# Kernel optimization log

Measured on AMD Instinct MI355X. Metric: run time of the kernel, lower is better.

## Reference

```python
import jax, jax.numpy as jnp
import numpy as np

D_MODEL = 1024
N_HEADS = 16
D_HEAD = D_MODEL // N_HEADS
BATCH = 4
SEQ = 2048
NEG_INF = -1e9  # finite large-negative; avoids NaNs on fully-masked rows under jit


def setup_inputs() -> dict:
    key = jax.random.key(0)
    ks = jax.random.split(key, 10)
    xav = np.sqrt(6.0 / (D_MODEL + D_MODEL))  # xavier_uniform bound
    def w(k):
        return jax.random.uniform(k, (D_MODEL, D_MODEL), jnp.float32, -xav, xav)
    return {
        "x": jax.random.normal(ks[0], (BATCH, SEQ, D_MODEL), jnp.float32),
        "attention_mask": jnp.tril(jnp.ones((SEQ, SEQ), jnp.int32)),  # causal: 0 => masked
        "key_padding_mask": jnp.zeros((BATCH, SEQ), jnp.bool_),  # True => masked
        "Wq": w(ks[1]), "bq": jnp.zeros((D_MODEL,), jnp.float32),
        "Wk": w(ks[2]), "bk": jnp.zeros((D_MODEL,), jnp.float32),
        "Wv": w(ks[3]), "bv": jnp.zeros((D_MODEL,), jnp.float32),
        "Wo": w(ks[4]), "bo": jnp.zeros((D_MODEL,), jnp.float32),
    }


def reference(x, attention_mask, key_padding_mask, Wq, bq, Wk, bk, Wv, bv, Wo, bo):
    b, s, d = x.shape
    scale = 1.0 / np.sqrt(D_HEAD)
    # torch Linear: x @ W.T + b
    def proj(W, bias):
        y = jnp.einsum('bsd,ed->bse', x, W) + bias
        return y.reshape(b, s, N_HEADS, D_HEAD).transpose(0, 2, 1, 3)  # (b,h,s,dh)
    q = proj(Wq, bq)
    k = proj(Wk, bk)
    v = proj(Wv, bv)
    scores = jnp.einsum('bhqd,bhkd->bhqk', q, k) * scale  # (b,h,s,s)
    scores = jnp.where(attention_mask[None, None] == 0, NEG_INF, scores)
    scores = jnp.where(key_padding_mask[:, None, None, :], NEG_INF, scores)
    attn = jax.nn.softmax(scores, axis=-1)
    out = jnp.einsum('bhqk,bhkd->bhqd', attn, v)  # (b,h,s,dh)
    out = out.transpose(0, 2, 1, 3).reshape(b, s, d)
    out = jnp.einsum('bsd,ed->bse', out, Wo) + bo
    return out
```

## Files before the change

kernel.cpp:

```cpp
#include <hip/hip_runtime.h>
#include <stdint.h>

typedef __bf16 bf16;
typedef __bf16 bf16x4 __attribute__((ext_vector_type(4)));
typedef __bf16 bf16x8 __attribute__((ext_vector_type(8)));
typedef float f32x4 __attribute__((ext_vector_type(4)));

typedef __attribute__((address_space(3))) uint32_t lds_u32_t;
typedef const __attribute__((address_space(1))) uint32_t glb_u32_t;

#define MFMA16(a, b, c) __builtin_amdgcn_mfma_f32_16x16x32_bf16((a), (b), (c), 0, 0, 0)

#if __has_builtin(__builtin_amdgcn_exp2f)
#define EXP2(x) __builtin_amdgcn_exp2f(x)
#else
#define EXP2(x) exp2f(x)
#endif

#define SEQ 2048
#define DMODEL 1024
#define NH 16
#define DH 64
#define MTOT 8192

#define KVB 64

#define VMW(n) asm volatile("s_waitcnt vmcnt(" #n ")" ::: "memory")
#define LGKM0()                                         \
  {                                                     \
    asm volatile("s_waitcnt lgkmcnt(0)" ::: "memory");  \
    __builtin_amdgcn_sched_barrier(0);                  \
  }
#define BARR()                                          \
  {                                                     \
    asm volatile("" ::: "memory");                      \
    __builtin_amdgcn_s_barrier();                       \
    asm volatile("" ::: "memory");                      \
  }

__global__ __launch_bounds__(256) void cvt_all(const float* __restrict__ x,
                                               const float* __restrict__ W0,
                                               const float* __restrict__ W1,
                                               const float* __restrict__ W2,
                                               const float* __restrict__ W3,
                                               bf16* __restrict__ xo, bf16* __restrict__ o0,
                                               bf16* __restrict__ o1, bf16* __restrict__ o2,
                                               bf16* __restrict__ o3) {
  int bid = blockIdx.x;
  const float* in;
  bf16* out;
  int within;
  if (bid < 8192) {
    in = x; out = xo; within = bid;
  } else {
    int r = bid - 8192;
    int wsel = r >> 10;
    within = r & 1023;
    switch (wsel) {
      case 0: in = W0; out = o0; break;
      case 1: in = W1; out = o1; break;
      case 2: in = W2; out = o2; break;
      default: in = W3; out = o3; break;
    }
  }
  int idx = (within * 256 + threadIdx.x) * 4;
  float4 v = *reinterpret_cast<const float4*>(in + idx);
  bf16x4 o;
  o[0] = (bf16)v.x; o[1] = (bf16)v.y; o[2] = (bf16)v.z; o[3] = (bf16)v.w;
  *reinterpret_cast<bf16x4*>(out + idx) = o;
}

static __device__ __forceinline__ void stage16(const bf16* g, const bf16* l) {
  __builtin_amdgcn_global_load_lds((glb_u32_t*)g, (lds_u32_t*)l, 16, 0, 0);
}

static __device__ __forceinline__ bf16x8 frag_ld(const bf16* base, int row, int col) {
  uint32_t byte = ((uint32_t)(row * 64 + col) * 2u) ^ (uint32_t)((row & 7) << 4);
  return *reinterpret_cast<const bf16x8*>(reinterpret_cast<const char*>(base) + byte);
}

static __device__ __forceinline__ void gemm128(const bf16* __restrict__ A,
                                               const bf16* __restrict__ B, int m0, int n0,
                                               int w, int lane, bf16* As, bf16* Bs,
                                               f32x4 acc[2][4]) {
  const int wm = w >> 1, wn = w & 1;
  const int cA = lane & 15, gA = lane >> 4;
  const int r8 = lane >> 3;
  const int csw = ((lane & 7) ^ r8) << 3;

#define SA_(kk, buf)                                                               \
  {                                                                                \
    _Pragma("unroll") for (int i_ = 0; i_ < 2; ++i_) {                             \
      int ci_ = w * 2 + i_;                                                        \
      stage16(A + (size_t)(m0 + ci_ * 8 + r8) * 1024 + (kk) + csw,                 \
              As + (buf)*8192 + ci_ * 512);                                        \
    }                                                                              \
  }
#define SB_(kk, buf)                                                               \
  {                                                                                \
    _Pragma("unroll") for (int i_ = 0; i_ < 2; ++i_) {                             \
      int ci_ = w * 2 + i_;                                                        \
      stage16(B + (size_t)(n0 + ci_ * 8 + r8) * 1024 + (kk) + csw,                 \
              Bs + (buf)*8192 + ci_ * 512);                                        \
    }                                                                              \
  }
#define CL3(x) ((x) < 16 ? (x) : (x)-3)
#define CL2(x) ((x) < 16 ? (x) : (x)-2)

  SA_(0, 0)
  SB_(0, 0)
  SA_(64, 1)
  VMW(2);
  BARR();

  int cur = 0, nxt = 1, nx2 = 2;
  bf16x8 aA[2], bB[4];

  for (int t = 0; t < 16; ++t) {
    const int bcur = t & 1;
    const bf16* Ac = As + cur * 8192;
    const bf16* Bc = Bs + bcur * 8192;

#pragma unroll
    for (int mi = 0; mi < 2; ++mi) aA[mi] = frag_ld(Ac, wm * 32 + mi * 16 + cA, gA * 8);
#pragma unroll
    for (int ni = 0; ni < 4; ++ni) bB[ni] = frag_ld(Bc, wn * 64 + ni * 16 + cA, gA * 8);

    SB_(CL2(t + 1) * 64, bcur ^ 1)

    BARR();
    LGKM0();
    __builtin_amdgcn_s_setprio(1);
#pragma unroll
    for (int mi = 0; mi < 2; ++mi)
#pragma unroll
      for (int ni = 0; ni < 4; ++ni) acc[mi][ni] = MFMA16(aA[mi], bB[ni], acc[mi][ni]);
    __builtin_amdgcn_s_setprio(0);
    BARR();

#pragma unroll
    for (int mi = 0; mi < 2; ++mi) aA[mi] = frag_ld(Ac, wm * 32 + mi * 16 + cA, 32 + gA * 8);
#pragma unroll
    for (int ni = 0; ni < 4; ++ni) bB[ni] = frag_ld(Bc, wn * 64 + ni * 16 + cA, 32 + gA * 8);

    SA_(CL3(t + 2) * 64, nx2)

    VMW(2);
    BARR();
    LGKM0();
    __builtin_amdgcn_s_setprio(1);
#pragma unroll
    for (int mi = 0; mi < 2; ++mi)
#pragma unroll
      for (int ni = 0; ni < 4; ++ni) acc[mi][ni] = MFMA16(aA[mi], bB[ni], acc[mi][ni]);
    __builtin_amdgcn_s_setprio(0);
    BARR();

    const int r_ = cur; cur = nxt; nxt = nx2; nx2 = r_;
  }
#undef SA_
#undef SB_
#undef CL3
#undef CL2
}

__global__ __launch_bounds__(512, 2) void qkv_gemm(
    const bf16* __restrict__ X, const bf16* __restrict__ Wq, const bf16* __restrict__ Wk,
    const bf16* __restrict__ Wv, const float* __restrict__ bq, const float* __restrict__ bk,
    const float* __restrict__ bv, bf16* __restrict__ Qo, bf16* __restrict__ Ko,
    bf16* __restrict__ Vt) {
  __shared__ bf16 As[3 * 8192];
  __shared__ bf16 Bs[2 * 8192];
  const int tid = threadIdx.x;
  const int w = tid >> 6, lane = tid & 63;
  const int ysel = blockIdx.y >> 3;
  const int n0 = (blockIdx.y & 7) * 128;
  const int m0 = blockIdx.x * 128;
  const bf16* W = (ysel == 0) ? Wq : ((ysel == 1) ? Wk : Wv);
  const float* bias = (ysel == 0) ? bq : ((ysel == 1) ? bk : bv);

  f32x4 acc[2][4];
  const f32x4 fz = {0.f, 0.f, 0.f, 0.f};
#pragma unroll
  for (int i = 0; i < 2; ++i)
#pragma unroll
    for (int j = 0; j < 4; ++j) acc[i][j] = fz;

  gemm128(X, W, m0, n0, w, lane, As, Bs, acc);

  const int wm = w >> 1, wn = w & 1;
  const int cA = lane & 15, gA = lane >> 4;

  if (ysel == 2) {
#pragma unroll
    for (int mi = 0; mi < 2; ++mi)
#pragma unroll
      for (int ni = 0; ni < 4; ++ni) {
        int e = n0 + wn * 64 + ni * 16 + cA;
        int h = e >> 6, dh = e & 63;
        int m = m0 + wm * 32 + mi * 16 + gA * 4;
        int b = m >> 11, s = m & 2047;
        float bb = bias[e];
        f32x4 v = acc[mi][ni];
        bf16x4 o;
        o[0] = (bf16)(v[0] + bb); o[1] = (bf16)(v[1] + bb);
        o[2] = (bf16)(v[2] + bb); o[3] = (bf16)(v[3] + bb);
        *reinterpret_cast<bf16x4*>(Vt + ((size_t)((b * NH + h) * DH + dh)) * SEQ + s) = o;
      }
  } else {
    bf16* dst = (ysel == 0) ? Qo : Ko;
    const float qs = (ysel == 0) ? 0.125f * 1.44269504f : 1.0f;
#pragma unroll
    for (int mi = 0; mi < 2; ++mi)
#pragma unroll
      for (int ni = 0; ni < 4; ++ni) {
        int e = n0 + wn * 64 + ni * 16 + cA;
        int h = e >> 6, dh = e & 63;
        int m = m0 + wm * 32 + mi * 16 + gA * 4;
        int b = m >> 11, s = m & 2047;
        float bb = bias[e];
        f32x4 v = acc[mi][ni];
        size_t base = ((size_t)(b * NH + h) * SEQ + s) * DH + dh;
#pragma unroll
        for (int j = 0; j < 4; ++j) dst[base + (size_t)j * DH] = (bf16)((v[j] + bb) * qs);
      }
  }
}

__global__ __launch_bounds__(512, 2) void out_gemm(const bf16* __restrict__ A,
                                                   const bf16* __restrict__ Wo,
                                                   const float* __restrict__ bo,
                                                   float* __restrict__ Out) {
  __shared__ bf16 As[3 * 8192];
  __shared__ bf16 Bs[2 * 8192];
  const int tid = threadIdx.x;
  const int w = tid >> 6, lane = tid & 63;
  const int m0 = blockIdx.x * 128;
  const int n0 = blockIdx.y * 128;

  f32x4 acc[2][4];
  const f32x4 fz = {0.f, 0.f, 0.f, 0.f};
#pragma unroll
  for (int i = 0; i < 2; ++i)
#pragma unroll
    for (int j = 0; j < 4; ++j) acc[i][j] = fz;

  gemm128(A, Wo, m0, n0, w, lane, As, Bs, acc);

  const int wm = w >> 1, wn = w & 1;
  const int cA = lane & 15, gA = lane >> 4;
#pragma unroll
  for (int mi = 0; mi < 2; ++mi)
#pragma unroll
    for (int ni = 0; ni < 4; ++ni) {
      int e = n0 + wn * 64 + ni * 16 + cA;
      int m = m0 + wm * 32 + mi * 16 + gA * 4;
      float bb = bo[e];
      f32x4 v = acc[mi][ni];
#pragma unroll
      for (int j = 0; j < 4; ++j) Out[(size_t)(m + j) * DMODEL + e] = v[j] + bb;
    }
}

__global__ __launch_bounds__(256, 3) void flash_attn(const bf16* __restrict__ Q,
                                                     const bf16* __restrict__ K,
                                                     const bf16* __restrict__ Vt,
                                                     bf16* __restrict__ O) {
  __shared__ bf16 Ks[2][KVB * DH];
  __shared__ bf16 Vs[2][KVB * DH];
  __shared__ bf16 Plds[4 * 2048];
  const int tid = threadIdx.x;
  const int w = tid >> 6, lane = tid & 63;
  const int bh = blockIdx.x;
  const int qt = 15 - (int)blockIdx.y;
  const int cA = lane & 15, gA = lane >> 4;
  const int l8 = lane & 7, r8 = lane >> 3;
  const int sb = lane & 48;

  const bf16* Qp = Q + (size_t)bh * SEQ * DH;
  const bf16* Kp = K + (size_t)bh * SEQ * DH;
  const bf16* Vp = Vt + (size_t)bh * DH * SEQ;
  const int b = bh >> 4, h = bh & 15;

  const uint32_t swz = (uint32_t)(cA & 7) << 4;
  const uint32_t lo0 = (uint32_t)cA * 128 + (((uint32_t)gA * 16) ^ swz);
  const uint32_t lo1 = (uint32_t)cA * 128 + ((64u + (uint32_t)gA * 16) ^ swz);
  char* pb = (char*)Plds + w * 4096;

#define STAGE_K(dst, kv)                                                          \
  {                                                                               \
    _Pragma("unroll") for (int i = 0; i < 2; ++i) {                               \
      int ci = w * 2 + i;                                                         \
      int r = ci * 8 + r8;                                                        \
      int c = ((l8 ^ (r & 7)) << 3);                                              \
      stage16(Kp + (size_t)((kv) + r) * DH + c, (dst) + ci * 512);                \
    }                                                                             \
  }
#define STAGE_V(dst, kv)                                                          \
  {                                                                               \
    _Pragma("unroll") for (int i = 0; i < 2; ++i) {                               \
      int ci = w * 2 + i;                                                         \
      int r = ci * 8 + r8;                                                        \
      int c = ((l8 ^ (r & 7)) << 3);                                              \
      stage16(Vp + (size_t)r * SEQ + (kv) + c, (dst) + ci * 512);                 \
    }                                                                             \
  }

  const f32x4 fz = {0.f, 0.f, 0.f, 0.f};

  const int nt = 2 * qt + 2;
  const int q0w = qt * 128 + w * 32;
  const int qmax = q0w + 31;

  bf16x8 qf[2][2];
#pragma unroll
  for (int qp = 0; qp < 2; ++qp) {
    qf[qp][0] = *reinterpret_cast<const bf16x8*>(Qp + (size_t)(q0w + qp * 16 + cA) * DH + gA * 8);
    qf[qp][1] =
        *reinterpret_cast<const bf16x8*>(Qp + (size_t)(q0w + qp * 16 + cA) * DH + 32 + gA * 8);
  }

  f32x4 o_acc[2][4];
#pragma unroll
  for (int qp = 0; qp < 2; ++qp)
#pragma unroll
    for (int dt = 0; dt < 4; ++dt) o_acc[qp][dt] = fz;
  float m_s[2] = {-1e30f, -1e30f}, l_s[2] = {0.f, 0.f};

  STAGE_K(Ks[0], 0)
  STAGE_V(Vs[0], 0)
  VMW(2);
  BARR();

  int cur = 0;
  for (int it = 0; it < nt; ++it) {
    const int kv = it * KVB;
    const int kvn = (it + 1 < nt) ? (kv + KVB) : kv;
    STAGE_K(Ks[cur ^ 1], kvn)
    STAGE_V(Vs[cur ^ 1], kvn)

    const bool active = (kv <= qmax);
    f32x4 s[4][2];
    if (active) {
      const char* kc = (const char*)&Ks[cur][0];
      bf16x8 kfr[2][2];
#pragma unroll
      for (int kt = 0; kt < 2; ++kt) {
        kfr[kt][0] = *reinterpret_cast<const bf16x8*>(kc + lo0 + kt * 2048);
        kfr[kt][1] = *reinterpret_cast<const bf16x8*>(kc + lo1 + kt * 2048);
      }
      LGKM0();
      __builtin_amdgcn_s_setprio(1);
#pragma unroll
      for (int kt = 0; kt < 2; ++kt)
#pragma unroll
        for (int qp = 0; qp < 2; ++qp) {
          s[kt][qp] = MFMA16(kfr[kt][0], qf[qp][0], fz);
          s[kt][qp] = MFMA16(kfr[kt][1], qf[qp][1], s[kt][qp]);
        }
      __builtin_amdgcn_s_setprio(0);
#pragma unroll
      for (int kt = 0; kt < 2; ++kt) {
        kfr[kt][0] = *reinterpret_cast<const bf16x8*>(kc + lo0 + (kt + 2) * 2048);
        kfr[kt][1] = *reinterpret_cast<const bf16x8*>(kc + lo1 + (kt + 2) * 2048);
      }
      LGKM0();
      __builtin_amdgcn_s_setprio(1);
#pragma unroll
      for (int kt = 0; kt < 2; ++kt)
#pragma unroll
        for (int qp = 0; qp < 2; ++qp) {
          s[kt + 2][qp] = MFMA16(kfr[kt][0], qf[qp][0], fz);
          s[kt + 2][qp] = MFMA16(kfr[kt][1], qf[qp][1], s[kt + 2][qp]);
        }
      __builtin_amdgcn_s_setprio(0);

#pragma unroll
      for (int qp = 0; qp < 2; ++qp) {
        if (kv + 63 > q0w + qp * 16) {
          const int q = q0w + qp * 16 + cA;
#pragma unroll
          for (int kt = 0; kt < 4; ++kt) {
            const int kb = kv + kt * 16 + gA * 4;
#pragma unroll
            for (int j = 0; j < 4; ++j)
              if (kb + j > q) s[kt][qp][j] = -1e30f;
          }
        }
      }

#pragma unroll
      for (int qp = 0; qp < 2; ++qp) {
        float ra = fmaxf(fmaxf(s[0][qp][0], s[0][qp][1]), s[0][qp][2]);
        ra = fmaxf(fmaxf(ra, s[0][qp][3]), s[1][qp][0]);
        ra = fmaxf(fmaxf(ra, s[1][qp][1]), s[1][qp][2]);
        float rb = fmaxf(fmaxf(s[2][qp][0], s[2][qp][1]), s[2][qp][2]);
        rb = fmaxf(fmaxf(rb, s[2][qp][3]), s[3][qp][0]);
        rb = fmaxf(fmaxf(rb, s[3][qp][1]), s[3][qp][2]);
        float r = fmaxf(fmaxf(ra, s[1][qp][3]), fmaxf(rb, s[3][qp][3]));
        r = fmaxf(r, __shfl_xor(r, 16));
        r = fmaxf(r, __shfl_xor(r, 32));

        const float mo = m_s[qp];
        float mn = mo;
        if (!__all(r <= mo + 12.0f)) {
          mn = fmaxf(mo, r);
          m_s[qp] = mn;
          const float scl = EXP2(mo - mn);
          float sclr[4];
#pragma unroll
          for (int j = 0; j < 4; ++j) sclr[j] = __shfl(scl, sb | (4 * gA + j));
#pragma unroll
          for (int dt = 0; dt < 4; ++dt) {
            f32x4 t = o_acc[qp][dt];
            t[0] *= sclr[0]; t[1] *= sclr[1]; t[2] *= sclr[2]; t[3] *= sclr[3];
            o_acc[qp][dt] = t;
          }
          l_s[qp] *= scl;
        }

        float rs = 0.f;
#pragma unroll
        for (int kt = 0; kt < 4; ++kt) {
          float p0 = EXP2(s[kt][qp][0] - mn);
          float p1 = EXP2(s[kt][qp][1] - mn);
          float p2 = EXP2(s[kt][qp][2] - mn);
          float p3 = EXP2(s[kt][qp][3] - mn);
          s[kt][qp][0] = p0; s[kt][qp][1] = p1; s[kt][qp][2] = p2; s[kt][qp][3] = p3;
          rs += (p0 + p1) + (p2 + p3);
        }
        rs += __shfl_xor(rs, 16);
        rs += __shfl_xor(rs, 32);
        l_s[qp] += rs;

#pragma unroll
        for (int kt = 0; kt < 4; ++kt) {
          bf16x4 t;
          t[0] = (bf16)s[kt][qp][0]; t[1] = (bf16)s[kt][qp][1];
          t[2] = (bf16)s[kt][qp][2]; t[3] = (bf16)s[kt][qp][3];
          *reinterpret_cast<bf16x4*>(
              pb + (qp * 16 + cA) * 128 + (((uint32_t)(kt * 32 + gA * 8)) ^ swz)) = t;
        }
      }
    }

    VMW(4);
    BARR();

    if (active) {
      bf16x8 pf[2][2];
#pragma unroll
      for (int qp = 0; qp < 2; ++qp) {
        pf[qp][0] = *reinterpret_cast<const bf16x8*>(
            pb + (qp * 16 + cA) * 128 + (((uint32_t)(gA * 16)) ^ swz));
        pf[qp][1] = *reinterpret_cast<const bf16x8*>(
            pb + (qp * 16 + cA) * 128 + (((uint32_t)(64 + gA * 16)) ^ swz));
      }
      const char* vc = (const char*)&Vs[cur][0];
      __builtin_amdgcn_s_setprio(1);
#pragma unroll
      for (int dt = 0; dt < 4; ++dt) {
        bf16x8 vf0 = *reinterpret_cast<const bf16x8*>(vc + lo0 + dt * 2048);
        bf16x8 vf1 = *reinterpret_cast<const bf16x8*>(vc + lo1 + dt * 2048);
#pragma unroll
        for (int qp = 0; qp < 2; ++qp) {
          o_acc[qp][dt] = MFMA16(pf[qp][0], vf0, o_acc[qp][dt]);
          o_acc[qp][dt] = MFMA16(pf[qp][1], vf1, o_acc[qp][dt]);
        }
      }
      __builtin_amdgcn_s_setprio(0);
    }

    VMW(2);
    BARR();
    cur ^= 1;
  }

  VMW(0);

#pragma unroll
  for (int qp = 0; qp < 2; ++qp) {
    const float li = 1.0f / l_s[qp];
    float lrow[4];
#pragma unroll
    for (int j = 0; j < 4; ++j) lrow[j] = __shfl(li, sb | (4 * gA + j));
#pragma unroll
    for (int dt = 0; dt < 4; ++dt) {
      const int dh = dt * 16 + cA;
#pragma unroll
      for (int j = 0; j < 4; ++j) {
        const int srow = q0w + qp * 16 + gA * 4 + j;
        O[((size_t)(b * SEQ + srow)) * DMODEL + h * DH + dh] =
            (bf16)(o_acc[qp][dt][j] * lrow[j]);
      }
    }
  }
#undef STAGE_K
#undef STAGE_V
}

extern "C" void kernel_launch(void* const* d_in, const int* in_sizes, int n_in, void* d_out,
                              int out_size, void* d_ws, size_t ws_size, hipStream_t stream) {
  const float* x = (const float*)d_in[0];
  const float* Wq = (const float*)d_in[3];
  const float* bq = (const float*)d_in[4];
  const float* Wk = (const float*)d_in[5];
  const float* bk = (const float*)d_in[6];
  const float* Wv = (const float*)d_in[7];
  const float* bv = (const float*)d_in[8];
  const float* Wo = (const float*)d_in[9];
  const float* bo = (const float*)d_in[10];
  float* out = (float*)d_out;

  char* ws = (char*)d_ws;
  bf16* xb = (bf16*)(ws + 0);
  bf16* wqb = (bf16*)(ws + 16777216);
  bf16* wkb = (bf16*)(ws + 18874368);
  bf16* wvb = (bf16*)(ws + 20971520);
  bf16* wob = (bf16*)(ws + 23068672);
  bf16* Qb = (bf16*)(ws + 25165824);
  bf16* Kb = (bf16*)(ws + 41943040);
  bf16* Vt = (bf16*)(ws + 58720256);
  bf16* Ab = xb;

  cvt_all<<<12288, 256, 0, stream>>>(x, Wq, Wk, Wv, Wo, xb, wqb, wkb, wvb, wob);

  qkv_gemm<<<dim3(64, 24), 512, 0, stream>>>(xb, wqb, wkb, wvb, bq, bk, bv, Qb, Kb, Vt);
  flash_attn<<<dim3(64, 16), 256, 0, stream>>>(Qb, Kb, Vt, Ab);
  out_gemm<<<dim3(64, 8), 512, 0, stream>>>(Ab, wob, bo, out);
}
```

Baseline: 159.7 us.

## Pair causal q-tiles per attention block and cut barriers in GEMM loop

The GEMM main loop loads both k-halves of fragments at once and issues both next-stage copies together, leaving one barrier per iteration instead of several. The GEMM launch bounds request more blocks per CU, which may constrain registers. The attention kernel processes two complementary causal query tiles per block to balance work across a halved grid. It also drops the intermediate barrier between softmax and PV, waiting fully on loads instead. The risks are register pressure and spills from the larger fragment arrays and tighter bounds, and less load/compute overlap from full vmcnt waits.

Result: slower. 163.1 us (+2.1%).

```diff
diff --git a/kernel.cpp b/kernel.cpp
--- a/kernel.cpp
+++ b/kernel.cpp
@@ -114,7 +114,7 @@
   BARR();
 
   int cur = 0, nxt = 1, nx2 = 2;
-  bf16x8 aA[2], bB[4];
+  bf16x8 aA[2][2], bB[4][2];
 
   for (int t = 0; t < 16; ++t) {
     const int bcur = t & 1;
@@ -122,38 +122,31 @@
     const bf16* Bc = Bs + bcur * 8192;
 
 #pragma unroll
-    for (int mi = 0; mi < 2; ++mi) aA[mi] = frag_ld(Ac, wm * 32 + mi * 16 + cA, gA * 8);
-#pragma unroll
-    for (int ni = 0; ni < 4; ++ni) bB[ni] = frag_ld(Bc, wn * 64 + ni * 16 + cA, gA * 8);
+    for (int mi = 0; mi < 2; ++mi)
+#pragma unroll
+      for (int ks = 0; ks < 2; ++ks)
+        aA[mi][ks] = frag_ld(Ac, wm * 32 + mi * 16 + cA, ks * 32 + gA * 8);
+#pragma unroll
+    for (int ni = 0; ni < 4; ++ni)
+#pragma unroll
+      for (int ks = 0; ks < 2; ++ks)
+        bB[ni][ks] = frag_ld(Bc, wn * 64 + ni * 16 + cA, ks * 32 + gA * 8);
 
     SB_(CL2(t + 1) * 64, bcur ^ 1)
-
-    BARR();
+    SA_(CL3(t + 2) * 64, nx2)
+
     LGKM0();
     __builtin_amdgcn_s_setprio(1);
 #pragma unroll
     for (int mi = 0; mi < 2; ++mi)
 #pragma unroll
-      for (int ni = 0; ni < 4; ++ni) acc[mi][ni] = MFMA16(aA[mi], bB[ni], acc[mi][ni]);
+      for (int ni = 0; ni < 4; ++ni) {
+        acc[mi][ni] = MFMA16(aA[mi][0], bB[ni][0], acc[mi][ni]);
+        acc[mi][ni] = MFMA16(aA[mi][1], bB[ni][1], acc[mi][ni]);
+      }
     __builtin_amdgcn_s_setprio(0);
-    BARR();
-
-#pragma unroll
-    for (int mi = 0; mi < 2; ++mi) aA[mi] = frag_ld(Ac, wm * 32 + mi * 16 + cA, 32 + gA * 8);
-#pragma unroll
-    for (int ni = 0; ni < 4; ++ni) bB[ni] = frag_ld(Bc, wn * 64 + ni * 16 + cA, 32 + gA * 8);
-
-    SA_(CL3(t + 2) * 64, nx2)
 
     VMW(2);
-    BARR();
-    LGKM0();
-    __builtin_amdgcn_s_setprio(1);
-#pragma unroll
-    for (int mi = 0; mi < 2; ++mi)
-#pragma unroll
-      for (int ni = 0; ni < 4; ++ni) acc[mi][ni] = MFMA16(aA[mi], bB[ni], acc[mi][ni]);
-    __builtin_amdgcn_s_setprio(0);
     BARR();
 
     const int r_ = cur; cur = nxt; nxt = nx2; nx2 = r_;
@@ -164,7 +157,7 @@
 #undef CL2
 }
 
-__global__ __launch_bounds__(512, 2) void qkv_gemm(
+__global__ __launch_bounds__(512, 4) void qkv_gemm(
     const bf16* __restrict__ X, const bf16* __restrict__ Wq, const bf16* __restrict__ Wk,
     const bf16* __restrict__ Wv, const float* __restrict__ bq, const float* __restrict__ bk,
     const float* __restrict__ bv, bf16* __restrict__ Qo, bf16* __restrict__ Ko,
@@ -227,7 +220,7 @@
   }
 }
 
-__global__ __launch_bounds__(512, 2) void out_gemm(const bf16* __restrict__ A,
+__global__ __launch_bounds__(512, 4) void out_gemm(const bf16* __restrict__ A,
                                                    const bf16* __restrict__ Wo,
                                                    const float* __restrict__ bo,
                                                    float* __restrict__ Out) {
@@ -272,7 +265,7 @@
   const int tid = threadIdx.x;
   const int w = tid >> 6, lane = tid & 63;
   const int bh = blockIdx.x;
-  const int qt = 15 - (int)blockIdx.y;
+  const int y = blockIdx.y;
   const int cA = lane & 15, gA = lane >> 4;
   const int l8 = lane & 7, r8 = lane >> 3;
   const int sb = lane & 48;
@@ -308,192 +301,190 @@
 
   const f32x4 fz = {0.f, 0.f, 0.f, 0.f};
 
-  const int nt = 2 * qt + 2;
-  const int q0w = qt * 128 + w * 32;
-  const int qmax = q0w + 31;
-
-  bf16x8 qf[2][2];
-#pragma unroll
-  for (int qp = 0; qp < 2; ++qp) {
-    qf[qp][0] = *reinterpret_cast<const bf16x8*>(Qp + (size_t)(q0w + qp * 16 + cA) * DH + gA * 8);
-    qf[qp][1] =
-        *reinterpret_cast<const bf16x8*>(Qp + (size_t)(q0w + qp * 16 + cA) * DH + 32 + gA * 8);
-  }
-
-  f32x4 o_acc[2][4];
-#pragma unroll
-  for (int qp = 0; qp < 2; ++qp)
-#pragma unroll
-    for (int dt = 0; dt < 4; ++dt) o_acc[qp][dt] = fz;
-  float m_s[2] = {-1e30f, -1e30f}, l_s[2] = {0.f, 0.f};
-
-  STAGE_K(Ks[0], 0)
-  STAGE_V(Vs[0], 0)
-  VMW(2);
-  BARR();
-
-  int cur = 0;
-  for (int it = 0; it < nt; ++it) {
-    const int kv = it * KVB;
-    const int kvn = (it + 1 < nt) ? (kv + KVB) : kv;
-    STAGE_K(Ks[cur ^ 1], kvn)
-    STAGE_V(Vs[cur ^ 1], kvn)
-
-    const bool active = (kv <= qmax);
-    f32x4 s[4][2];
-    if (active) {
-      const char* kc = (const char*)&Ks[cur][0];
-      bf16x8 kfr[2][2];
-#pragma unroll
-      for (int kt = 0; kt < 2; ++kt) {
-        kfr[kt][0] = *reinterpret_cast<const bf16x8*>(kc + lo0 + kt * 2048);
-        kfr[kt][1] = *reinterpret_cast<const bf16x8*>(kc + lo1 + kt * 2048);
+  for (int phase = 0; phase < 2; ++phase) {
+    const int qt = phase ? y : (15 - y);
+    const int nt = 2 * qt + 2;
+    const int q0w = qt * 128 + w * 32;
+    const int qmax = q0w + 31;
+
+    bf16x8 qf[2][2];
+#pragma unroll
+    for (int qp = 0; qp < 2; ++qp) {
+      qf[qp][0] =
+          *reinterpret_cast<const bf16x8*>(Qp + (size_t)(q0w + qp * 16 + cA) * DH + gA * 8);
+      qf[qp][1] =
+          *reinterpret_cast<const bf16x8*>(Qp + (size_t)(q0w + qp * 16 + cA) * DH + 32 + gA * 8);
+    }
+
+    f32x4 o_acc[2][4];
+#pragma unroll
+    for (int qp = 0; qp < 2; ++qp)
+#pragma unroll
+      for (int dt = 0; dt < 4; ++dt) o_acc[qp][dt] = fz;
+    float m_s[2] = {-1e30f, -1e30f}, l_s[2] = {0.f, 0.f};
+
+    STAGE_K(Ks[0], 0)
+    STAGE_V(Vs[0], 0)
+    VMW(0);
+    BARR();
+
+    int cur = 0;
+    for (int it = 0; it < nt; ++it) {
+      const int kv = it * KVB;
+      const int kvn = (it + 1 < nt) ? (kv + KVB) : kv;
+      STAGE_K(Ks[cur ^ 1], kvn)
+      STAGE_V(Vs[cur ^ 1], kvn)
+
+      const bool active = (kv <= qmax);
+      if (active) {
+        const char* kc = (const char*)&Ks[cur][0];
+        f32x4 s[4][2];
+        bf16x8 kfr[2][2];
+#pragma unroll
+        for (int kt = 0; kt < 2; ++kt) {
+          kfr[kt][0] = *reinterpret_cast<const bf16x8*>(kc + lo0 + kt * 2048);
+          kfr[kt][1] = *reinterpret_cast<const bf16x8*>(kc + lo1 + kt * 2048);
+        }
+        LGKM0();
+        __builtin_amdgcn_s_setprio(1);
+#pragma unroll
+        for (int kt = 0; kt < 2; ++kt)
+#pragma unroll
+          for (int qp = 0; qp < 2; ++qp) {
+            s[kt][qp] = MFMA16(kfr[kt][0], qf[qp][0], fz);
+            s[kt][qp] = MFMA16(kfr[kt][1], qf[qp][1], s[kt][qp]);
+          }
+        __builtin_amdgcn_s_setprio(0);
+#pragma unroll
+        for (int kt = 0; kt < 2; ++kt) {
+          kfr[kt][0] = *reinterpret_cast<const bf16x8*>(kc + lo0 + (kt + 2) * 2048);
+          kfr[kt][1] = *reinterpret_cast<const bf16x8*>(kc + lo1 + (kt + 2) * 2048);
+        }
+        LGKM0();
+        __builtin_amdgcn_s_setprio(1);
+#pragma unroll
+        for (int kt = 0; kt < 2; ++kt)
+#pragma unroll
+          for (int qp = 0; qp < 2; ++qp) {
+            s[kt + 2][qp] = MFMA16(kfr[kt][0], qf[qp][0], fz);
+            s[kt + 2][qp] = MFMA16(kfr[kt][1], qf[qp][1], s[kt + 2][qp]);
+          }
+        __builtin_amdgcn_s_setprio(0);
+
+#pragma unroll
+        for (int qp = 0; qp < 2; ++qp) {
+          if (kv + 63 > q0w + qp * 16) {
+            const int q = q0w + qp * 16 + cA;
+#pragma unroll
+            for (int kt = 0; kt < 4; ++kt) {
+              const int kb = kv + kt * 16 + gA * 4;
+#pragma unroll
+              for (int j = 0; j < 4; ++j)
+                if (kb + j > q) s[kt][qp][j] = -1e30f;
+            }
+          }
+        }
+
+#pragma unroll
+        for (int qp = 0; qp < 2; ++qp) {
+          float ra = fmaxf(fmaxf(s[0][qp][0], s[0][qp][1]), s[0][qp][2]);
+          ra = fmaxf(fmaxf(ra, s[0][qp][3]), s[1][qp][0]);
+          ra = fmaxf(fmaxf(ra, s[1][qp][1]), s[1][qp][2]);
+          float rb = fmaxf(fmaxf(s[2][qp][0], s[2][qp][1]), s[2][qp][2]);
+          rb = fmaxf(fmaxf(rb, s[2][qp][3]), s[3][qp][0]);
+          rb = fmaxf(fmaxf(rb, s[3][qp][1]), s[3][qp][2]);
+          float r = fmaxf(fmaxf(ra, s[1][qp][3]), fmaxf(rb, s[3][qp][3]));
+          r = fmaxf(r, __shfl_xor(r, 16));
+          r = fmaxf(r, __shfl_xor(r, 32));
+
+          const float mo = m_s[qp];
+          float mn = mo;
+          if (!__all(r <= mo + 12.0f)) {
+            mn = fmaxf(mo, r);
+            m_s[qp] = mn;
+            const float scl = EXP2(mo - mn);
+            float sclr[4];
+#pragma unroll
+            for (int j = 0; j < 4; ++j) sclr[j] = __shfl(scl, sb | (4 * gA + j));
+#pragma unroll
+            for (int dt = 0; dt < 4; ++dt) {
+              f32x4 t = o_acc[qp][dt];
+              t[0] *= sclr[0]; t[1] *= sclr[1]; t[2] *= sclr[2]; t[3] *= sclr[3];
+              o_acc[qp][dt] = t;
+            }
+            l_s[qp] *= scl;
+          }
+
+          float rs = 0.f;
+#pragma unroll
+          for (int kt = 0; kt < 4; ++kt) {
+            float p0 = EXP2(s[kt][qp][0] - mn);
+            float p1 = EXP2(s[kt][qp][1] - mn);
+            float p2 = EXP2(s[kt][qp][2] - mn);
+            float p3 = EXP2(s[kt][qp][3] - mn);
+            s[kt][qp][0] = p0; s[kt][qp][1] = p1; s[kt][qp][2] = p2; s[kt][qp][3] = p3;
+            rs += (p0 + p1) + (p2 + p3);
+          }
+          rs += __shfl_xor(rs, 16);
+          rs += __shfl_xor(rs, 32);
+          l_s[qp] += rs;
+
+#pragma unroll
+          for (int kt = 0; kt < 4; ++kt) {
+            bf16x4 t;
+            t[0] = (bf16)s[kt][qp][0]; t[1] = (bf16)s[kt][qp][1];
+            t[2] = (bf16)s[kt][qp][2]; t[3] = (bf16)s[kt][qp][3];
+            *reinterpret_cast<bf16x4*>(
+                pb + (qp * 16 + cA) * 128 + (((uint32_t)(kt * 32 + gA * 8)) ^ swz)) = t;
+          }
+        }
+
+        bf16x8 pf[2][2];
+#pragma unroll
+        for (int qp = 0; qp < 2; ++qp) {
+          pf[qp][0] = *reinterpret_cast<const bf16x8*>(
+              pb + (qp * 16 + cA) * 128 + (((uint32_t)(gA * 16)) ^ swz));
+          pf[qp][1] = *reinterpret_cast<const bf16x8*>(
+              pb + (qp * 16 + cA) * 128 + (((uint32_t)(64 + gA * 16)) ^ swz));
+        }
+        const char* vc = (const char*)&Vs[cur][0];
+        __builtin_amdgcn_s_setprio(1);
+#pragma unroll
+        for (int dt = 0; dt < 4; ++dt) {
+          bf16x8 vf0 = *reinterpret_cast<const bf16x8*>(vc + lo0 + dt * 2048);
+          bf16x8 vf1 = *reinterpret_cast<const bf16x8*>(vc + lo1 + dt * 2048);
+#pragma unroll
+          for (int qp = 0; qp < 2; ++qp) {
+            o_acc[qp][dt] = MFMA16(pf[qp][0], vf0, o_acc[qp][dt]);
+            o_acc[qp][dt] = MFMA16(pf[qp][1], vf1, o_acc[qp][dt]);
+          }
+        }
+        __builtin_amdgcn_s_setprio(0);
       }
-      LGKM0();
-      __builtin_amdgcn_s_setprio(1);
-#pragma unroll
-      for (int kt = 0; kt < 2; ++kt)
-#pragma unroll
-        for (int qp = 0; qp < 2; ++qp) {
-          s[kt][qp] = MFMA16(kfr[kt][0], qf[qp][0], fz);
-          s[kt][qp] = MFMA16(kfr[kt][1], qf[qp][1], s[kt][qp]);
-        }
-      __builtin_amdgcn_s_setprio(0);
-#pragma unroll
-      for (int kt = 0; kt < 2; ++kt) {
-        kfr[kt][0] = *reinterpret_cast<const bf16x8*>(kc + lo0 + (kt + 2) * 2048);
-        kfr[kt][1] = *reinterpret_cast<const bf16x8*>(kc + lo1 + (kt + 2) * 2048);
-      }
-      LGKM0();
-      __builtin_amdgcn_s_setprio(1);
-#pragma unroll
-      for (int kt = 0; kt < 2; ++kt)
-#pragma unroll
-        for (int qp = 0; qp < 2; ++qp) {
-          s[kt + 2][qp] = MFMA16(kfr[kt][0], qf[qp][0], fz);
-          s[kt + 2][qp] = MFMA16(kfr[kt][1], qf[qp][1], s[kt + 2][qp]);
-        }
-      __builtin_amdgcn_s_setprio(0);
-
-#pragma unroll
-      for (int qp = 0; qp < 2; ++qp) {
-        if (kv + 63 > q0w + qp * 16) {
-          const int q = q0w + qp * 16 + cA;
-#pragma unroll
-          for (int kt = 0; kt < 4; ++kt) {
-            const int kb = kv + kt * 16 + gA * 4;
-#pragma unroll
-            for (int j = 0; j < 4; ++j)
-              if (kb + j > q) s[kt][qp][j] = -1e30f;
-          }
-        }
-      }
-
-#pragma unroll
-      for (int qp = 0; qp < 2; ++qp) {
-        float ra = fmaxf(fmaxf(s[0][qp][0], s[0][qp][1]), s[0][qp][2]);
-        ra = fmaxf(fmaxf(ra, s[0][qp][3]), s[1][qp][0]);
-        ra = fmaxf(fmaxf(ra, s[1][qp][1]), s[1][qp][2]);
-        float rb = fmaxf(fmaxf(s[2][qp][0], s[2][qp][1]), s[2][qp][2]);
-        rb = fmaxf(fmaxf(rb, s[2][qp][3]), s[3][qp][0]);
-        rb = fmaxf(fmaxf(rb, s[3][qp][1]), s[3][qp][2]);
-        float r = fmaxf(fmaxf(ra, s[1][qp][3]), fmaxf(rb, s[3][qp][3]));
-        r = fmaxf(r, __shfl_xor(r, 16));
-        r = fmaxf(r, __shfl_xor(r, 32));
-
-        const float mo = m_s[qp];
-        float mn = mo;
-        if (!__all(r <= mo + 12.0f)) {
-          mn = fmaxf(mo, r);
-          m_s[qp] = mn;
-          const float scl = EXP2(mo - mn);
-          float sclr[4];
-#pragma unroll
-          for (int j = 0; j < 4; ++j) sclr[j] = __shfl(scl, sb | (4 * gA + j));
-#pragma unroll
-          for (int dt = 0; dt < 4; ++dt) {
-            f32x4 t = o_acc[qp][dt];
-            t[0] *= sclr[0]; t[1] *= sclr[1]; t[2] *= sclr[2]; t[3] *= sclr[3];
-            o_acc[qp][dt] = t;
-          }
-          l_s[qp] *= scl;
-        }
-
-        float rs = 0.f;
-#pragma unroll
-        for (int kt = 0; kt < 4; ++kt) {
-          float p0 = EXP2(s[kt][qp][0] - mn);
-          float p1 = EXP2(s[kt][qp][1] - mn);
-          float p2 = EXP2(s[kt][qp][2] - mn);
-          float p3 = EXP2(s[kt][qp][3] - mn);
-          s[kt][qp][0] = p0; s[kt][qp][1] = p1; s[kt][qp][2] = p2; s[kt][qp][3] = p3;
-          rs += (p0 + p1) + (p2 + p3);
-        }
-        rs += __shfl_xor(rs, 16);
-        rs += __shfl_xor(rs, 32);
-        l_s[qp] += rs;
-
-#pragma unroll
-        for (int kt = 0; kt < 4; ++kt) {
-          bf16x4 t;
-          t[0] = (bf16)s[kt][qp][0]; t[1] = (bf16)s[kt][qp][1];
-          t[2] = (bf16)s[kt][qp][2]; t[3] = (bf16)s[kt][qp][3];
-          *reinterpret_cast<bf16x4*>(
-              pb + (qp * 16 + cA) * 128 + (((uint32_t)(kt * 32 + gA * 8)) ^ swz)) = t;
+
+      VMW(0);
+      BARR();
+      cur ^= 1;
+    }
+
+#pragma unroll
+    for (int qp = 0; qp < 2; ++qp) {
+      const float li = 1.0f / l_s[qp];
+      float lrow[4];
+#pragma unroll
+      for (int j = 0; j < 4; ++j) lrow[j] = __shfl(li, sb | (4 * gA + j));
+#pragma unroll
+      for (int dt = 0; dt < 4; ++dt) {
+        const int dh = dt * 16 + cA;
+#pragma unroll
+        for (int j = 0; j < 4; ++j) {
+          const int srow = q0w + qp * 16 + gA * 4 + j;
+          O[((size_t)(b * SEQ + srow)) * DMODEL + h * DH + dh] =
+              (bf16)(o_acc[qp][dt][j] * lrow[j]);
         }
       }
     }
-
-    VMW(4);
     BARR();
-
-    if (active) {
-      bf16x8 pf[2][2];
-#pragma unroll
-      for (int qp = 0; qp < 2; ++qp) {
-        pf[qp][0] = *reinterpret_cast<const bf16x8*>(
-            pb + (qp * 16 + cA) * 128 + (((uint32_t)(gA * 16)) ^ swz));
-        pf[qp][1] = *reinterpret_cast<const bf16x8*>(
-            pb + (qp * 16 + cA) * 128 + (((uint32_t)(64 + gA * 16)) ^ swz));
-      }
-      const char* vc = (const char*)&Vs[cur][0];
-      __builtin_amdgcn_s_setprio(1);
-#pragma unroll
-      for (int dt = 0; dt < 4; ++dt) {
-        bf16x8 vf0 = *reinterpret_cast<const bf16x8*>(vc + lo0 + dt * 2048);
-        bf16x8 vf1 = *reinterpret_cast<const bf16x8*>(vc + lo1 + dt * 2048);
-#pragma unroll
-        for (int qp = 0; qp < 2; ++qp) {
-          o_acc[qp][dt] = MFMA16(pf[qp][0], vf0, o_acc[qp][dt]);
-          o_acc[qp][dt] = MFMA16(pf[qp][1], vf1, o_acc[qp][dt]);
-        }
-      }
-      __builtin_amdgcn_s_setprio(0);
-    }
-
-    VMW(2);
-    BARR();
-    cur ^= 1;
-  }
-
-  VMW(0);
-
-#pragma unroll
-  for (int qp = 0; qp < 2; ++qp) {
-    const float li = 1.0f / l_s[qp];
-    float lrow[4];
-#pragma unroll
-    for (int j = 0; j < 4; ++j) lrow[j] = __shfl(li, sb | (4 * gA + j));
-#pragma unroll
-    for (int dt = 0; dt < 4; ++dt) {
-      const int dh = dt * 16 + cA;
-#pragma unroll
-      for (int j = 0; j < 4; ++j) {
-        const int srow = q0w + qp * 16 + gA * 4 + j;
-        O[((size_t)(b * SEQ + srow)) * DMODEL + h * DH + dh] =
-            (bf16)(o_acc[qp][dt][j] * lrow[j]);
-      }
-    }
   }
 #undef STAGE_K
 #undef STAGE_V
@@ -526,6 +517,6 @@
   cvt_all<<<12288, 256, 0, stream>>>(x, Wq, Wk, Wv, Wo, xb, wqb, wkb, wvb, wob);
 
   qkv_gemm<<<dim3(64, 24), 512, 0, stream>>>(xb, wqb, wkb, wvb, bq, bk, bv, Qb, Kb, Vt);
-  flash_attn<<<dim3(64, 16), 256, 0, stream>>>(Qb, Kb, Vt, Ab);
+  flash_attn<<<dim3(64, 8), 256, 0, stream>>>(Qb, Kb, Vt, Ab);
   out_gemm<<<dim3(64, 8), 512, 0, stream>>>(Ab, wob, bo, out);
 }
```
